# Performance work log

Hardware: AMD Instinct MI355X
Metric: run time of the kernel (lower is better)

The kernel has to match this reference:

```python
import jax, jax.numpy as jnp
import numpy as np


def setup_inputs() -> dict:
    key = jax.random.key(0)
    k1, k2 = jax.random.split(key)
    N, M, D = 16384, 16384, 3
    target_pc = jax.random.normal(k1, (N, D), dtype=jnp.float32)
    output_pc = jax.random.normal(k2, (M, D), dtype=jnp.float32)
    return {"target_pc": target_pc, "output_pc": output_pc}


def _min_dist_sum(a, b):
    # sum over rows of min_j ||a_i - b_j||, via the norm-expansion trick
    sq_a = jnp.sum(a * a, axis=1, keepdims=True)          # [N,1]
    sq_b = jnp.sum(b * b, axis=1, keepdims=True).T        # [1,M]
    sq_dst = sq_a - 2.0 * (a @ b.T) + sq_b                # [N,M]
    dist = jnp.sqrt(jnp.maximum(sq_dst, 0.0))
    return jnp.sum(jnp.min(dist, axis=1))


def reference(target_pc, output_pc):
    loss_a_to_b = _min_dist_sum(output_pc, target_pc)
    loss_b_to_a = _min_dist_sum(target_pc, output_pc)
    return (loss_a_to_b + loss_b_to_a) / 1000.0
```

## Files before the change

### kernel.cpp

```cpp
#include <hip/hip_runtime.h>
#include <cfloat>

#define NPTS 16384
#define C_CHUNKS 32
#define CHUNK (NPTS / C_CHUNKS)
#define NA 4

__global__ __launch_bounds__(256) void chamfer_min_kernel(
    const float* __restrict__ target, const float* __restrict__ output,
    int* __restrict__ minsq)
{
    __shared__ float4 bs[CHUNK];

    const int dir = blockIdx.z;
    const float* __restrict__ A = dir ? target : output;
    const float* __restrict__ B = dir ? output : target;

    const int j0 = blockIdx.y * CHUNK;
    for (int k = threadIdx.x; k < CHUNK; k += 256) {
        int j = j0 + k;
        float x = B[3 * j], y = B[3 * j + 1], z = B[3 * j + 2];
        bs[k] = make_float4(-2.f * x, -2.f * y, -2.f * z,
                            fmaf(x, x, fmaf(y, y, z * z)));
    }

    const int i0 = blockIdx.x * (256 * NA) + threadIdx.x;
    float ax[NA], ay[NA], az[NA], sqa[NA], m[NA];
    #pragma unroll
    for (int k = 0; k < NA; ++k) {
        int i = i0 + k * 256;
        ax[k] = A[3 * i]; ay[k] = A[3 * i + 1]; az[k] = A[3 * i + 2];
        sqa[k] = fmaf(ax[k], ax[k], fmaf(ay[k], ay[k], az[k] * az[k]));
        m[k] = FLT_MAX;
    }
    __syncthreads();

    #pragma unroll 4
    for (int j = 0; j < CHUNK; ++j) {
        float4 p = bs[j];
        #pragma unroll
        for (int k = 0; k < NA; ++k) {
            float s = fmaf(ax[k], p.x, fmaf(ay[k], p.y, fmaf(az[k], p.z, p.w)));
            m[k] = fminf(m[k], s);
        }
    }

    #pragma unroll
    for (int k = 0; k < NA; ++k)
        atomicMin(&minsq[dir * NPTS + i0 + k * 256], __float_as_int(m[k] + sqa[k]));
}

__global__ __launch_bounds__(256) void reduce_kernel(
    const int* __restrict__ minsq, float* __restrict__ out)
{
    int t = blockIdx.x * 256 + threadIdx.x;
    float s = 0.f;
    for (int k = t; k < 2 * NPTS; k += gridDim.x * 256) {
        float v = __int_as_float(minsq[k]);
        s += sqrtf(fmaxf(v, 0.f));
    }
    for (int off = 32; off; off >>= 1) s += __shfl_down(s, off, 64);
    __shared__ float partial[4];
    int wid = threadIdx.x >> 6;
    if ((threadIdx.x & 63) == 0) partial[wid] = s;
    __syncthreads();
    if (threadIdx.x == 0) {
        float tot = (partial[0] + partial[1]) + (partial[2] + partial[3]);
        atomicAdd(out, tot * 0.001f);
    }
}

extern "C" void kernel_launch(void* const* d_in, const int* in_sizes, int n_in,
                              void* d_out, int out_size, void* d_ws, size_t ws_size,
                              hipStream_t stream) {
    const float* target = (const float*)d_in[0];
    const float* output = (const float*)d_in[1];
    float* out = (float*)d_out;

    int* minsq = (int*)d_ws;

    hipMemsetAsync(minsq, 0x7F, 2 * NPTS * sizeof(int), stream);
    hipMemsetAsync(out, 0, sizeof(float), stream);

    chamfer_min_kernel<<<dim3(NPTS / (256 * NA), C_CHUNKS, 2), 256, 0, stream>>>(
        target, output, minsq);
    reduce_kernel<<<32, 256, 0, stream>>>(minsq, out);
}
```

Baseline: 101.3 us.

## Pack inner loop with v2f FMAs and fuse reduction via last-block pattern

```diff
diff --git a/kernel.cpp b/kernel.cpp
--- a/kernel.cpp
+++ b/kernel.cpp
@@ -5,12 +5,16 @@
 #define C_CHUNKS 32
 #define CHUNK (NPTS / C_CHUNKS)
 #define NA 4
+#define NBLOCKS (2 * C_CHUNKS * NPTS / (256 * NA))
+#define CTR_INIT 0x7F7F7F7Fu
 
-__global__ __launch_bounds__(256) void chamfer_min_kernel(
+typedef float v2f __attribute__((ext_vector_type(2)));
+
+__global__ __launch_bounds__(256) void chamfer_kernel(
     const float* __restrict__ target, const float* __restrict__ output,
-    int* __restrict__ minsq)
+    int* __restrict__ minsq, float* __restrict__ out)
 {
-    __shared__ float4 bs[CHUNK];
+    __shared__ float bsx[CHUNK], bsy[CHUNK], bsz[CHUNK], bsw[CHUNK];
 
     const int dir = blockIdx.z;
     const float* __restrict__ A = dir ? target : output;
@@ -20,53 +24,63 @@
     for (int k = threadIdx.x; k < CHUNK; k += 256) {
         int j = j0 + k;
         float x = B[3 * j], y = B[3 * j + 1], z = B[3 * j + 2];
-        bs[k] = make_float4(-2.f * x, -2.f * y, -2.f * z,
-                            fmaf(x, x, fmaf(y, y, z * z)));
+        bsx[k] = -2.f * x; bsy[k] = -2.f * y; bsz[k] = -2.f * z;
+        bsw[k] = fmaf(x, x, fmaf(y, y, z * z));
     }
 
     const int i0 = blockIdx.x * (256 * NA) + threadIdx.x;
-    float ax[NA], ay[NA], az[NA], sqa[NA], m[NA];
+    v2f ax[NA], ay[NA], az[NA];
+    float sqa[NA], m[NA];
     #pragma unroll
     for (int k = 0; k < NA; ++k) {
         int i = i0 + k * 256;
-        ax[k] = A[3 * i]; ay[k] = A[3 * i + 1]; az[k] = A[3 * i + 2];
-        sqa[k] = fmaf(ax[k], ax[k], fmaf(ay[k], ay[k], az[k] * az[k]));
+        float x = A[3 * i], y = A[3 * i + 1], z = A[3 * i + 2];
+        ax[k] = (v2f){x, x}; ay[k] = (v2f){y, y}; az[k] = (v2f){z, z};
+        sqa[k] = fmaf(x, x, fmaf(y, y, z * z));
         m[k] = FLT_MAX;
     }
     __syncthreads();
 
-    #pragma unroll 4
-    for (int j = 0; j < CHUNK; ++j) {
-        float4 p = bs[j];
+    #pragma unroll 2
+    for (int j = 0; j < CHUNK; j += 2) {
+        v2f px = *(const v2f*)&bsx[j];
+        v2f py = *(const v2f*)&bsy[j];
+        v2f pz = *(const v2f*)&bsz[j];
+        v2f pw = *(const v2f*)&bsw[j];
         #pragma unroll
         for (int k = 0; k < NA; ++k) {
-            float s = fmaf(ax[k], p.x, fmaf(ay[k], p.y, fmaf(az[k], p.z, p.w)));
-            m[k] = fminf(m[k], s);
+            v2f s = __builtin_elementwise_fma(ax[k], px,
+                      __builtin_elementwise_fma(ay[k], py,
+                        __builtin_elementwise_fma(az[k], pz, pw)));
+            m[k] = fminf(m[k], fminf(s.x, s.y));
         }
     }
 
     #pragma unroll
     for (int k = 0; k < NA; ++k)
         atomicMin(&minsq[dir * NPTS + i0 + k * 256], __float_as_int(m[k] + sqa[k]));
-}
 
-__global__ __launch_bounds__(256) void reduce_kernel(
-    const int* __restrict__ minsq, float* __restrict__ out)
-{
-    int t = blockIdx.x * 256 + threadIdx.x;
-    float s = 0.f;
-    for (int k = t; k < 2 * NPTS; k += gridDim.x * 256) {
-        float v = __int_as_float(minsq[k]);
-        s += sqrtf(fmaxf(v, 0.f));
+    __threadfence();
+    __shared__ bool amLast;
+    if (threadIdx.x == 0) {
+        unsigned old = atomicAdd((unsigned*)&minsq[2 * NPTS], 1u);
+        amLast = (old == CTR_INIT + NBLOCKS - 1);
     }
-    for (int off = 32; off; off >>= 1) s += __shfl_down(s, off, 64);
-    __shared__ float partial[4];
-    int wid = threadIdx.x >> 6;
-    if ((threadIdx.x & 63) == 0) partial[wid] = s;
     __syncthreads();
-    if (threadIdx.x == 0) {
-        float tot = (partial[0] + partial[1]) + (partial[2] + partial[3]);
-        atomicAdd(out, tot * 0.001f);
+    if (amLast) {
+        __threadfence();
+        float s = 0.f;
+        for (int k = threadIdx.x; k < 2 * NPTS; k += 256) {
+            int v = __hip_atomic_load(&minsq[k], __ATOMIC_RELAXED,
+                                      __HIP_MEMORY_SCOPE_AGENT);
+            s += sqrtf(fmaxf(__int_as_float(v), 0.f));
+        }
+        for (int off = 32; off; off >>= 1) s += __shfl_down(s, off, 64);
+        __shared__ float partial[4];
+        if ((threadIdx.x & 63) == 0) partial[threadIdx.x >> 6] = s;
+        __syncthreads();
+        if (threadIdx.x == 0)
+            out[0] = (partial[0] + partial[1] + partial[2] + partial[3]) * 0.001f;
     }
 }
 
@@ -76,13 +90,10 @@
     const float* target = (const float*)d_in[0];
     const float* output = (const float*)d_in[1];
     float* out = (float*)d_out;
-
     int* minsq = (int*)d_ws;
 
-    hipMemsetAsync(minsq, 0x7F, 2 * NPTS * sizeof(int), stream);
-    hipMemsetAsync(out, 0, sizeof(float), stream);
+    hipMemsetAsync(minsq, 0x7F, (2 * NPTS + 1) * sizeof(int), stream);
 
-    chamfer_min_kernel<<<dim3(NPTS / (256 * NA), C_CHUNKS, 2), 256, 0, stream>>>(
-        target, output, minsq);
-    reduce_kernel<<<32, 256, 0, stream>>>(minsq, out);
+    chamfer_kernel<<<dim3(NPTS / (256 * NA), C_CHUNKS, 2), 256, 0, stream>>>(
+        target, output, minsq, out);
 }
```

After: 175.3 us. +73.1%, slower.
